# Kernel tuning notes

Hardware: AMD Instinct MI355X
Metric: run time of the kernel (lower is better)

Reference implementation:

```python
import jax, jax.numpy as jnp
import numpy as np

B, S, D = 2, 2048, 1024
E, K, F = 64, 6, 1408
DFF = 4096
N = B * S
CAP = 768
Z_LOSS_W = 1e-6
MOE_SCALE = 0.5  # 1/(1 + (num_shared_experts > 0))


def setup_inputs() -> dict:
    key = jax.random.key(0)
    ks = jax.random.split(key, 7)
    x = jax.random.normal(ks[0], (B, S, D), jnp.float32)
    router_w = jax.random.normal(ks[1], (E, D), jnp.float32) * 0.01
    experts_w12 = jax.random.normal(ks[2], (E, D, 2 * F), jnp.float32) * 0.011
    experts_w3 = jax.random.normal(ks[3], (E, F, D), jnp.float32) * 0.011
    gate_w = jax.random.normal(ks[4], (DFF, D), jnp.float32) * 0.011
    up_w = jax.random.normal(ks[5], (DFF, D), jnp.float32) * 0.011
    down_w = jax.random.normal(ks[6], (D, DFF), jnp.float32) * 0.011
    return {"x": x, "router_w": router_w, "experts_w12": experts_w12,
            "experts_w3": experts_w3, "gate_w": gate_w, "up_w": up_w,
            "down_w": down_w}


def reference(x, router_w, experts_w12, experts_w3, gate_w, up_w, down_w):
    b, s, d = x.shape
    h = x.reshape(-1, d)                    # [N, D]
    n = h.shape[0]

    # ---- router (fp32) ----
    logits = h @ router_w.T                 # [N, E]
    scores = jax.nn.sigmoid(logits)
    z_loss = jnp.mean(logits ** 2) * Z_LOSS_W
    # expert_bias defaults to zeros -> selection on scores directly
    _, topk_idx = jax.lax.top_k(scores, K)  # [N, K]
    topk_idx = jnp.clip(topk_idx, 0, E - 1)
    topk_logits = jnp.take_along_axis(logits, topk_idx, axis=1)
    gating = jax.nn.softmax(topk_logits, axis=-1).astype(jnp.bfloat16)  # [N, K]

    # ---- shared expert (dense SwiGLU) ----
    shared = (jax.nn.silu(h @ gate_w.T) * (h @ up_w.T)) @ down_w.T  # [N, D]

    # ---- dispatch: sort token-expert pairs by expert, scatter into padded buffer ----
    flat_idx = topk_idx.reshape(-1)                     # [N*K]
    order = jnp.argsort(flat_idx)
    expert_sorted = flat_idx[order]                     # [N*K]
    token_ids = jnp.repeat(jnp.arange(n), K)[order]     # source token per pair
    counts = jnp.bincount(flat_idx, length=E)
    starts = jnp.concatenate([jnp.zeros((1,), counts.dtype), jnp.cumsum(counts)[:-1]])
    intra = jnp.arange(n * K) - starts[expert_sorted]   # slot within expert
    valid = intra < CAP
    dest = jnp.where(valid, expert_sorted * CAP + intra, E * CAP)  # overflow -> trash row

    grouped = h[token_ids]                              # [N*K, D]
    padded = jnp.zeros((E * CAP + 1, d), h.dtype).at[dest].set(grouped)
    padded = padded[:-1].reshape(E, CAP, d)             # [E, CAP, D]

    # ---- per-expert grouped GEMM (SwiGLU) ----
    h12 = jnp.einsum('ecd,edf->ecf', padded, experts_w12)   # [E, CAP, 2F]
    h1, h2 = jnp.split(h12, 2, axis=-1)
    act = jax.nn.silu(h1) * h2
    eout = jnp.einsum('ecf,efd->ecd', act, experts_w3)      # [E, CAP, D]

    # ---- combine: gather back and scatter-add into token order ----
    eout_flat = jnp.concatenate([eout.reshape(-1, d), jnp.zeros((1, d), eout.dtype)])
    full = eout_flat[dest]                              # [N*K, D]
    g_sorted = gating.reshape(-1)[order].astype(h.dtype)
    weighted = full * g_sorted[:, None]
    routed = jnp.zeros((n, d), h.dtype).at[token_ids].add(weighted)

    # eval mode: aux_loss = 0, route_scale = 1.0
    out = (shared + routed) * MOE_SCALE
    return out.reshape(b, s, d), z_loss
```

## Files before the change

### kernel.cpp

```cpp
#include <hip/hip_runtime.h>
#include <stdint.h>
#include <math.h>

#define NTOK 4096
#define DIM  1024
#define NEXP 64
#define KSEL 6
#define FF   1408
#define FF2  2816
#define DFFC 4096
#define CAPE 768

typedef __bf16 bf16x8 __attribute__((ext_vector_type(8)));
typedef float  f32x4  __attribute__((ext_vector_type(4)));

__device__ __forceinline__ float bf2f(uint32_t h) {
  union { uint32_t u; float f; } v; v.u = h << 16; return v.f;
}
__device__ __forceinline__ uint16_t f2bf(float f) {
  union { float f; uint32_t u; } v; v.f = f;
  return (uint16_t)((v.u + 0x7fffu + ((v.u >> 16) & 1u)) >> 16);
}
__device__ __forceinline__ uint32_t pk_bf16(float a, float b) {
  uint32_t r;
  asm("v_cvt_pk_bf16_f32 %0, %1, %2" : "=v"(r) : "v"(a), "v"(b));
  return r;
}
__device__ __forceinline__ int swzh(int r) { return ((r ^ (r >> 2)) & 7) << 3; }

__device__ __forceinline__ void load_lds16(const void* g, void* l) {
  __builtin_amdgcn_global_load_lds((const __attribute__((address_space(1))) void*)g,
                                   (__attribute__((address_space(3))) void*)l, 16, 0, 0);
}

__global__ __launch_bounds__(256) void router_kernel(const float* __restrict__ x,
                                                     const float* __restrict__ rw,
                                                     int* __restrict__ topk,
                                                     uint16_t* __restrict__ gating,
                                                     float* __restrict__ tokz,
                                                     uint16_t* __restrict__ hb) {
  __shared__ float hs[16 * DIM];
  __shared__ float lg[16][NEXP];
  const int tid = threadIdx.x;
  const int t0 = blockIdx.x * 16;
  const float4* xin = (const float4*)(x + (size_t)t0 * DIM);
  float4* hs4 = (float4*)hs;
  for (int i = tid; i < 16 * DIM / 4; i += 256) hs4[i] = xin[i];
  __syncthreads();
  {
    ushort4* hbo = (ushort4*)(hb + (size_t)t0 * DIM);
    for (int i = tid; i < 16 * DIM / 4; i += 256) {
      float4 v = hs4[i];
      ushort4 o;
      o.x = f2bf(v.x); o.y = f2bf(v.y); o.z = f2bf(v.z); o.w = f2bf(v.w);
      hbo[i] = o;
    }
  }
  const int e = tid >> 2, q = tid & 3;
  float part[16];
#pragma unroll
  for (int tt = 0; tt < 16; tt++) part[tt] = 0.f;
  const float4* rw4 = (const float4*)(rw + (size_t)e * DIM + q * 256);
  for (int i = 0; i < 64; i++) {
    float4 w = rw4[i];
#pragma unroll
    for (int tt = 0; tt < 16; tt++) {
      float4 h = *(const float4*)(hs + tt * DIM + q * 256 + i * 4);
      part[tt] += h.x * w.x + h.y * w.y + h.z * w.z + h.w * w.w;
    }
  }
#pragma unroll
  for (int tt = 0; tt < 16; tt++) {
    float v = part[tt];
    v += __shfl_xor(v, 1);
    v += __shfl_xor(v, 2);
    if (q == 0) lg[tt][e] = v;
  }
  __syncthreads();
  const int wid = tid >> 6, lane = tid & 63;
  for (int ti = 0; ti < 4; ti++) {
    int tt = wid * 4 + ti;
    float v = lg[tt][lane];
    float z = v * v;
#pragma unroll
    for (int off = 32; off; off >>= 1) z += __shfl_xor(z, off);
    float bv[KSEL]; int bi[KSEL];
#pragma unroll
    for (int s = 0; s < KSEL; s++) {
      float m = v; int mi = lane;
#pragma unroll
      for (int off = 32; off; off >>= 1) {
        float om = __shfl_xor(m, off); int oi = __shfl_xor(mi, off);
        if (om > m || (om == m && oi < mi)) { m = om; mi = oi; }
      }
      bv[s] = m; bi[s] = mi;
      if (lane == mi) v = -3.0e38f;
    }
    if (lane == 0) {
      int t = t0 + tt;
      tokz[t] = z;
      float mx = bv[0];
      float ex[KSEL], sum = 0.f;
#pragma unroll
      for (int s = 0; s < KSEL; s++) { ex[s] = expf(bv[s] - mx); sum += ex[s]; }
      float inv = 1.f / sum;
#pragma unroll
      for (int s = 0; s < KSEL; s++) {
        topk[t * KSEL + s] = bi[s];
        gating[t * KSEL + s] = f2bf(ex[s] * inv);
      }
    }
  }
}

__global__ __launch_bounds__(256) void zred_kernel(const float* __restrict__ tz,
                                                   float* __restrict__ out) {
  __shared__ float s[256];
  float a = 0.f;
  for (int i = threadIdx.x; i < NTOK; i += 256) a += tz[i];
  s[threadIdx.x] = a; __syncthreads();
  for (int st = 128; st; st >>= 1) {
    if (threadIdx.x < (unsigned)st) s[threadIdx.x] += s[threadIdx.x + st];
    __syncthreads();
  }
  if (threadIdx.x == 0) out[0] = s[0] * (1e-6f / ((float)NTOK * (float)NEXP));
}

__global__ __launch_bounds__(64) void dispatch_kernel(const int* __restrict__ topk,
                                                      int* __restrict__ dest,
                                                      int* __restrict__ invmap,
                                                      int* __restrict__ counts) {
  const int e = blockIdx.x;
  const int lane = threadIdx.x;
  int base = 0;
  for (int it = 0; it < (NTOK * KSEL) / 64; it++) {
    int p = it * 64 + lane;
    int ex = topk[p];
    bool m = (ex == e);
    unsigned long long mask = __ballot(m);
    if (m) {
      int intra = base + __popcll(mask & ((1ull << lane) - 1ull));
      if (intra < CAPE) {
        dest[p] = e * CAPE + intra;
        invmap[e * CAPE + intra] = p / KSEL;
      } else {
        dest[p] = -1;
      }
    }
    base += __popcll(mask);
  }
  if (lane == 0) counts[e] = base < CAPE ? base : CAPE;
}

#define BM 128
#define BN 128
#define BKK 64

template<int EPI, int BSRC, bool IND, bool REMAP>
__global__ __launch_bounds__(256, 3) void gemm_f(const uint16_t* __restrict__ A,
                                                 const float* __restrict__ B,
                                                 const float* __restrict__ B2,
                                                 void* __restrict__ C,
                                                 const int* __restrict__ invmap,
                                                 const int* __restrict__ counts,
                                                 int K, int lda, int ldb, int ldc,
                                                 long long strideA, long long strideB,
                                                 long long strideC, int grouped,
                                                 int nM, int nN) {
  const int per = gridDim.x >> 3;
  const int w = ((int)blockIdx.x & 7) * per + ((int)blockIdx.x >> 3);
  const int mi = w % nM;
  const int q1 = w / nM;
  const int ni = q1 % nN;
  const int e  = q1 / nN;
  int cnt = 1 << 30;
  if (grouped) {
    cnt = counts[e];
    if (mi * BM >= cnt) return;
  }
  const int bm0 = mi * BM, bn0 = ni * BN;
  const uint16_t* Ab = A + (size_t)e * strideA;
  const float* Bb = B + (size_t)e * strideB;
  __shared__ alignas(16) uint16_t sA[2][BM * BKK];
  __shared__ alignas(16) uint16_t sB[BN * BKK];
  const int tid = threadIdx.x, wid = tid >> 6, lane = tid & 63;

  const int sa = tid >> 3;
  const int colk = (((tid & 7) ^ ((sa ^ (sa >> 2)) & 7)) * 8);
  const uint16_t* ap[4];
#pragma unroll
  for (int i = 0; i < 4; i++) {
    int row = i * 32 + sa;
    int ar = bm0 + row;
    if constexpr (IND) {
      int cr = ar < cnt ? ar : (cnt - 1);
      ar = invmap[e * CAPE + cr];
    }
    ap[i] = Ab + (size_t)ar * lda + colk;
  }

  const float* bpa = nullptr;
  const float* bpb = nullptr;
  if constexpr (BSRC == 1) {
    const int kc = (tid & 15) * 4;
    bpa = Bb + (size_t)(bn0 + (tid >> 4)) * ldb + kc;
  } else if constexpr (BSRC == 3) {
    const int kc = (tid & 15) * 4;
    const int gcol = (bn0 >> 1) + (tid >> 4);
    bpa = B  + (size_t)gcol * ldb + kc;
    bpb = B2 + (size_t)gcol * ldb + kc;
  } else {
    const int n0 = 4 * (tid & 31);
    int vn0 = bn0 + n0;
    int ng0;
    if constexpr (REMAP) {
      int blk = vn0 >> 5, lo = vn0 & 31;
      ng0 = blk * 16 + (lo & 15) + (lo < 16 ? 0 : FF);
    } else {
      ng0 = vn0;
    }
    bpa = Bb + (size_t)(4 * (tid >> 5)) * ldb + ng0;
  }

  auto loadB = [&](f32x4 (&v)[8]) {
    if constexpr (BSRC == 1) {
#pragma unroll
      for (int it = 0; it < 8; it++)
        v[it] = *(const f32x4*)(bpa + (size_t)(it * 16) * ldb);
      bpa += BKK;
    } else if constexpr (BSRC == 3) {
#pragma unroll
      for (int it = 0; it < 8; it++) {
        const float* s = (it & 1) ? bpb : bpa;
        v[it] = *(const f32x4*)(s + (size_t)((it >> 1) * 16) * ldb);
      }
      bpa += BKK; bpb += BKK;
    } else {
#pragma unroll
      for (int i2 = 0; i2 < 2; i2++)
#pragma unroll
        for (int j = 0; j < 4; j++)
          v[i2 * 4 + j] = *(const f32x4*)(bpa + (size_t)(32 * i2 + j) * ldb);
      bpa += (size_t)BKK * ldb;
    }
  };
  auto issueA = [&](int buf) {
#pragma unroll
    for (int i = 0; i < 4; i++) {
      load_lds16(ap[i], sA[buf] + i * 2048 + wid * 512);
      ap[i] += BKK;
    }
  };
  auto writeB = [&](f32x4 (&v)[8]) {
    if constexpr (BSRC == 1 || BSRC == 3) {
      const int kc = (tid & 15) * 4;
#pragma unroll
      for (int it = 0; it < 8; it++) {
        int nr = (tid >> 4) + it * 16;
        uint2 p;
        p.x = pk_bf16(v[it][0], v[it][1]);
        p.y = pk_bf16(v[it][2], v[it][3]);
        *(uint2*)(sB + nr * BKK + (kc ^ swzh(nr))) = p;
      }
    } else {
      const int n0 = 4 * (tid & 31);
#pragma unroll
      for (int i2 = 0; i2 < 2; i2++) {
        int kk0 = 4 * (tid >> 5) + 32 * i2;
#pragma unroll
        for (int c = 0; c < 4; c++) {
          int nr = n0 + c;
          uint2 p;
          p.x = pk_bf16(v[i2 * 4 + 0][c], v[i2 * 4 + 1][c]);
          p.y = pk_bf16(v[i2 * 4 + 2][c], v[i2 * 4 + 3][c]);
          *(uint2*)(sB + nr * BKK + (kk0 ^ swzh(nr))) = p;
        }
      }
    }
  };

  f32x4 zero = {0.f, 0.f, 0.f, 0.f};
  f32x4 acc[4][4];
#pragma unroll
  for (int i = 0; i < 4; i++)
#pragma unroll
    for (int j = 0; j < 4; j++) acc[i][j] = zero;
  const int wm = wid >> 1, wn = wid & 1;

  f32x4 bv[8];
  issueA(0);
  loadB(bv);

  const int T = K / BKK;
  for (int t = 0; t < T; t++) {
    const int cur = t & 1, nb = cur ^ 1;
    const bool more = (t + 1 < T);
    if (more) issueA(nb);
    writeB(bv);
    if (more) loadB(bv);
    asm volatile("s_waitcnt lgkmcnt(0)" ::: "memory");
    __builtin_amdgcn_sched_barrier(0);
    __builtin_amdgcn_s_barrier();
    __builtin_amdgcn_sched_barrier(0);
#pragma unroll
    for (int ks = 0; ks < 2; ks++) {
      const int kb = ks * 32 + (lane >> 4) * 8;
      bf16x8 af[4], bfr[4];
#pragma unroll
      for (int f = 0; f < 4; f++) {
        int rowA = wm * 64 + f * 16 + (lane & 15);
        af[f] = *(const bf16x8*)(sA[cur] + rowA * BKK + (kb ^ swzh(rowA)));
      }
#pragma unroll
      for (int f = 0; f < 4; f++) {
        int rowB = wn * 64 + f * 16 + (lane & 15);
        bfr[f] = *(const bf16x8*)(sB + rowB * BKK + (kb ^ swzh(rowB)));
      }
#pragma unroll
      for (int fm = 0; fm < 4; fm++)
#pragma unroll
        for (int fn = 0; fn < 4; fn++)
          acc[fm][fn] = __builtin_amdgcn_mfma_f32_16x16x32_bf16(af[fm], bfr[fn],
                                                                acc[fm][fn], 0, 0, 0);
    }
    __builtin_amdgcn_sched_barrier(0);
    __builtin_amdgcn_s_barrier();
    __builtin_amdgcn_sched_barrier(0);
  }

  const int lr = (lane >> 4) * 4, lc = lane & 15;
  if constexpr (EPI == 2) {
    uint16_t* outp = (uint16_t*)C + (size_t)e * strideC;
#pragma unroll
    for (int fm = 0; fm < 4; fm++) {
#pragma unroll
      for (int fp = 0; fp < 2; fp++) {
        f32x4 g = acc[fm][2 * fp], u = acc[fm][2 * fp + 1];
        int fcol = (bn0 >> 1) + wn * 32 + fp * 16 + lc;
#pragma unroll
        for (int j = 0; j < 4; j++) {
          int r = bm0 + wm * 64 + fm * 16 + lr + j;
          float gv = g[j];
          float sv = (gv / (1.f + expf(-gv))) * u[j];
          outp[(size_t)r * ldc + fcol] = f2bf(sv);
        }
      }
    }
  } else if constexpr (EPI == 1) {
    float* outp = (float*)C + (size_t)e * strideC;
#pragma unroll
    for (int fm = 0; fm < 4; fm++)
#pragma unroll
      for (int fn = 0; fn < 4; fn++) {
        int col = bn0 + wn * 64 + fn * 16 + lc;
#pragma unroll
        for (int j = 0; j < 4; j++) {
          int r = bm0 + wm * 64 + fm * 16 + lr + j;
          outp[(size_t)r * ldc + col] = acc[fm][fn][j];
        }
      }
  } else {
    uint16_t* outp = (uint16_t*)C + (size_t)e * strideC;
#pragma unroll
    for (int fm = 0; fm < 4; fm++)
#pragma unroll
      for (int fn = 0; fn < 4; fn++) {
        int col = bn0 + wn * 64 + fn * 16 + lc;
#pragma unroll
        for (int j = 0; j < 4; j++) {
          int r = bm0 + wm * 64 + fm * 16 + lr + j;
          outp[(size_t)r * ldc + col] = f2bf(acc[fm][fn][j]);
        }
      }
  }
}

__global__ __launch_bounds__(256) void combine_kernel(const float* __restrict__ shout,
                                                      const uint16_t* __restrict__ eout,
                                                      const int* __restrict__ dest,
                                                      const uint16_t* __restrict__ gating,
                                                      float* __restrict__ out) {
  const int t = blockIdx.x;
  const int d0 = threadIdx.x * 4;
  float4 s0 = *(const float4*)(shout + (size_t)t * DIM + d0);
  float4 s1 = *(const float4*)(shout + (size_t)NTOK * DIM + (size_t)t * DIM + d0);
  float rx = 0.f, ry = 0.f, rz = 0.f, rw = 0.f;
#pragma unroll
  for (int k = 0; k < KSEL; k++) {
    int dp = dest[t * KSEL + k];
    if (dp >= 0) {
      float gw = bf2f(gating[t * KSEL + k]);
      ushort4 ev = *(const ushort4*)(eout + (size_t)dp * DIM + d0);
      rx += gw * bf2f(ev.x);
      ry += gw * bf2f(ev.y);
      rz += gw * bf2f(ev.z);
      rw += gw * bf2f(ev.w);
    }
  }
  float4 o;
  o.x = (s0.x + s1.x + rx) * 0.5f;
  o.y = (s0.y + s1.y + ry) * 0.5f;
  o.z = (s0.z + s1.z + rz) * 0.5f;
  o.w = (s0.w + s1.w + rw) * 0.5f;
  *(float4*)(out + (size_t)t * DIM + d0) = o;
}

extern "C" void kernel_launch(void* const* d_in, const int* in_sizes, int n_in,
                              void* d_out, int out_size, void* d_ws, size_t ws_size,
                              hipStream_t stream) {
  (void)in_sizes; (void)n_in; (void)out_size; (void)ws_size;
  const float* x   = (const float*)d_in[0];
  const float* rw  = (const float*)d_in[1];
  const float* w12 = (const float*)d_in[2];
  const float* w3  = (const float*)d_in[3];
  const float* gw  = (const float*)d_in[4];
  const float* uw  = (const float*)d_in[5];
  const float* dw  = (const float*)d_in[6];
  float* out = (float*)d_out;

  char* ws = (char*)d_ws;
  size_t off = 0;
  auto alloc = [&](size_t sz) -> void* {
    void* p = ws + off;
    off += (sz + 255) & ~(size_t)255;
    return p;
  };
  uint16_t* HB    = (uint16_t*)alloc((size_t)NTOK * DIM * 2);
  uint16_t* S1    = (uint16_t*)alloc((size_t)NTOK * DFFC * 2);
  uint16_t* ACT   = (uint16_t*)alloc((size_t)NEXP * CAPE * FF * 2);
  uint16_t* EOUT  = (uint16_t*)alloc((size_t)NEXP * CAPE * DIM * 2);
  float* SHOUT    = (float*)alloc((size_t)2 * NTOK * DIM * 4);
  int* TOPKB      = (int*)alloc((size_t)NTOK * KSEL * 4);
  uint16_t* GATING= (uint16_t*)alloc((size_t)NTOK * KSEL * 2);
  int* DEST       = (int*)alloc((size_t)NTOK * KSEL * 4);
  int* INVMAP     = (int*)alloc((size_t)NEXP * CAPE * 4);
  int* COUNTS     = (int*)alloc((size_t)NEXP * 4);
  float* TOKZ     = (float*)alloc((size_t)NTOK * 4);

  router_kernel<<<NTOK / 16, 256, 0, stream>>>(x, rw, TOPKB, GATING, TOKZ, HB);
  dispatch_kernel<<<NEXP, 64, 0, stream>>>(TOPKB, DEST, INVMAP, COUNTS);
  zred_kernel<<<1, 256, 0, stream>>>(TOKZ, out + (size_t)NTOK * DIM);

  gemm_f<2, 3, false, false><<<(NTOK / BM) * (2 * DFFC / BN), 256, 0, stream>>>(
      HB, gw, uw, S1, nullptr, nullptr, DIM, DIM, DIM, DFFC, 0, 0, 0, 0,
      NTOK / BM, 2 * DFFC / BN);
  gemm_f<1, 1, false, false><<<(NTOK / BM) * (DIM / BN) * 2, 256, 0, stream>>>(
      S1, dw, nullptr, SHOUT, nullptr, nullptr, DFFC / 2, DFFC, DFFC, DIM,
      DFFC / 2, DFFC / 2, (long long)NTOK * DIM, 0, NTOK / BM, DIM / BN);

  gemm_f<2, 2, true, true><<<(CAPE / BM) * (FF2 / BN) * NEXP, 256, 0, stream>>>(
      HB, w12, nullptr, ACT, INVMAP, COUNTS, DIM, DIM, FF2, FF,
      0, (long long)DIM * FF2, (long long)CAPE * FF, 1, CAPE / BM, FF2 / BN);
  gemm_f<0, 2, false, false><<<(CAPE / BM) * (DIM / BN) * NEXP, 256, 0, stream>>>(
      ACT, w3, nullptr, EOUT, nullptr, COUNTS, FF, FF, DIM, DIM,
      (long long)CAPE * FF, (long long)FF * DIM, (long long)CAPE * DIM, 1,
      CAPE / BM, DIM / BN);

  combine_kernel<<<NTOK, 256, 0, stream>>>(SHOUT, EOUT, DEST, GATING, out);
}
```

Measured before the change: 758.8 us.

## Double-buffer B tile in LDS and cut to one barrier per k-step

Doubles the shared-memory B tile so the next k-step's A and B tiles are written while the current one is consumed by MFMAs. B global loads now run two steps ahead, and each iteration ends with a single barrier that waits with a partial vmcnt instead of two full barriers. The aim is to hide global-load and LDS-write latency and remove one synchronization per iteration. The cost is 16KB more LDS per block and the removal of the minimum-occupancy hint, so the register budget and occupancy may change.

```diff
diff --git a/kernel.cpp b/kernel.cpp
--- a/kernel.cpp
+++ b/kernel.cpp
@@ -157,16 +157,16 @@
 #define BKK 64
 
 template<int EPI, int BSRC, bool IND, bool REMAP>
-__global__ __launch_bounds__(256, 3) void gemm_f(const uint16_t* __restrict__ A,
-                                                 const float* __restrict__ B,
-                                                 const float* __restrict__ B2,
-                                                 void* __restrict__ C,
-                                                 const int* __restrict__ invmap,
-                                                 const int* __restrict__ counts,
-                                                 int K, int lda, int ldb, int ldc,
-                                                 long long strideA, long long strideB,
-                                                 long long strideC, int grouped,
-                                                 int nM, int nN) {
+__global__ __launch_bounds__(256) void gemm_f(const uint16_t* __restrict__ A,
+                                              const float* __restrict__ B,
+                                              const float* __restrict__ B2,
+                                              void* __restrict__ C,
+                                              const int* __restrict__ invmap,
+                                              const int* __restrict__ counts,
+                                              int K, int lda, int ldb, int ldc,
+                                              long long strideA, long long strideB,
+                                              long long strideC, int grouped,
+                                              int nM, int nN) {
   const int per = gridDim.x >> 3;
   const int w = ((int)blockIdx.x & 7) * per + ((int)blockIdx.x >> 3);
   const int mi = w % nM;
@@ -182,7 +182,7 @@
   const uint16_t* Ab = A + (size_t)e * strideA;
   const float* Bb = B + (size_t)e * strideB;
   __shared__ alignas(16) uint16_t sA[2][BM * BKK];
-  __shared__ alignas(16) uint16_t sB[BN * BKK];
+  __shared__ alignas(16) uint16_t sB[2][BN * BKK];
   const int tid = threadIdx.x, wid = tid >> 6, lane = tid & 63;
 
   const int sa = tid >> 3;
@@ -251,7 +251,7 @@
       ap[i] += BKK;
     }
   };
-  auto writeB = [&](f32x4 (&v)[8]) {
+  auto writeB = [&](int buf, f32x4 (&v)[8]) {
     if constexpr (BSRC == 1 || BSRC == 3) {
       const int kc = (tid & 15) * 4;
 #pragma unroll
@@ -260,7 +260,7 @@
         uint2 p;
         p.x = pk_bf16(v[it][0], v[it][1]);
         p.y = pk_bf16(v[it][2], v[it][3]);
-        *(uint2*)(sB + nr * BKK + (kc ^ swzh(nr))) = p;
+        *(uint2*)(sB[buf] + nr * BKK + (kc ^ swzh(nr))) = p;
       }
     } else {
       const int n0 = 4 * (tid & 31);
@@ -273,7 +273,7 @@
           uint2 p;
           p.x = pk_bf16(v[i2 * 4 + 0][c], v[i2 * 4 + 1][c]);
           p.y = pk_bf16(v[i2 * 4 + 2][c], v[i2 * 4 + 3][c]);
-          *(uint2*)(sB + nr * BKK + (kk0 ^ swzh(nr))) = p;
+          *(uint2*)(sB[buf] + nr * BKK + (kk0 ^ swzh(nr))) = p;
         }
       }
     }
@@ -287,21 +287,26 @@
     for (int j = 0; j < 4; j++) acc[i][j] = zero;
   const int wm = wid >> 1, wn = wid & 1;
 
+  const int T = K / BKK;
   f32x4 bv[8];
   issueA(0);
   loadB(bv);
-
-  const int T = K / BKK;
+  writeB(0, bv);
+  if (T > 1) loadB(bv);
+  asm volatile("s_waitcnt lgkmcnt(0)" ::: "memory");
+  __builtin_amdgcn_sched_barrier(0);
+  __builtin_amdgcn_s_barrier();
+  __builtin_amdgcn_sched_barrier(0);
+
   for (int t = 0; t < T; t++) {
     const int cur = t & 1, nb = cur ^ 1;
-    const bool more = (t + 1 < T);
-    if (more) issueA(nb);
-    writeB(bv);
-    if (more) loadB(bv);
-    asm volatile("s_waitcnt lgkmcnt(0)" ::: "memory");
-    __builtin_amdgcn_sched_barrier(0);
-    __builtin_amdgcn_s_barrier();
-    __builtin_amdgcn_sched_barrier(0);
+    const bool more1 = (t + 1 < T);
+    const bool more2 = (t + 2 < T);
+    if (more1) {
+      issueA(nb);
+      writeB(nb, bv);
+    }
+    if (more2) loadB(bv);
 #pragma unroll
     for (int ks = 0; ks < 2; ks++) {
       const int kb = ks * 32 + (lane >> 4) * 8;
@@ -314,7 +319,7 @@
 #pragma unroll
       for (int f = 0; f < 4; f++) {
         int rowB = wn * 64 + f * 16 + (lane & 15);
-        bfr[f] = *(const bf16x8*)(sB + rowB * BKK + (kb ^ swzh(rowB)));
+        bfr[f] = *(const bf16x8*)(sB[cur] + rowB * BKK + (kb ^ swzh(rowB)));
       }
 #pragma unroll
       for (int fm = 0; fm < 4; fm++)
@@ -323,9 +328,16 @@
           acc[fm][fn] = __builtin_amdgcn_mfma_f32_16x16x32_bf16(af[fm], bfr[fn],
                                                                 acc[fm][fn], 0, 0, 0);
     }
-    __builtin_amdgcn_sched_barrier(0);
-    __builtin_amdgcn_s_barrier();
-    __builtin_amdgcn_sched_barrier(0);
+    if (more1) {
+      if (more2) {
+        asm volatile("s_waitcnt vmcnt(8) lgkmcnt(0)" ::: "memory");
+      } else {
+        asm volatile("s_waitcnt vmcnt(0) lgkmcnt(0)" ::: "memory");
+      }
+      __builtin_amdgcn_sched_barrier(0);
+      __builtin_amdgcn_s_barrier();
+      __builtin_amdgcn_sched_barrier(0);
+    }
   }
 
   const int lr = (lane >> 4) * 4, lc = lane & 15;
```

New measurement: 845.9 us. 1.11x slower.

## Merge shared and routed expert GEMMs into combined launches, fold z-loss into dispatch

Applied to the files above, without the earlier changes.

The shared-expert up GEMM and the routed-expert w12 GEMM now run in one launch, with the block index deciding which problem each block handles. The two down GEMMs are merged the same way. The z-loss reduction becomes an extra block of the dispatch kernel. This removes launch gaps and the tail underutilisation at the end of each GEMM, so the grouped GEMM's sparse and early-exiting blocks can overlap with dense shared-expert work. The cost is that both template bodies share one kernel's register budget and occupancy.

```diff
diff --git a/kernel.cpp b/kernel.cpp
--- a/kernel.cpp
+++ b/kernel.cpp
@@ -113,25 +113,22 @@
   }
 }
 
-__global__ __launch_bounds__(256) void zred_kernel(const float* __restrict__ tz,
-                                                   float* __restrict__ out) {
-  __shared__ float s[256];
-  float a = 0.f;
-  for (int i = threadIdx.x; i < NTOK; i += 256) a += tz[i];
-  s[threadIdx.x] = a; __syncthreads();
-  for (int st = 128; st; st >>= 1) {
-    if (threadIdx.x < (unsigned)st) s[threadIdx.x] += s[threadIdx.x + st];
-    __syncthreads();
-  }
-  if (threadIdx.x == 0) out[0] = s[0] * (1e-6f / ((float)NTOK * (float)NEXP));
-}
-
 __global__ __launch_bounds__(64) void dispatch_kernel(const int* __restrict__ topk,
                                                       int* __restrict__ dest,
                                                       int* __restrict__ invmap,
-                                                      int* __restrict__ counts) {
+                                                      int* __restrict__ counts,
+                                                      const float* __restrict__ tz,
+                                                      float* __restrict__ zout) {
+  const int lane = threadIdx.x;
+  if (blockIdx.x == NEXP) {
+    float a = 0.f;
+    for (int i = lane; i < NTOK; i += 64) a += tz[i];
+#pragma unroll
+    for (int off = 32; off; off >>= 1) a += __shfl_xor(a, off);
+    if (lane == 0) zout[0] = a * (1e-6f / ((float)NTOK * (float)NEXP));
+    return;
+  }
   const int e = blockIdx.x;
-  const int lane = threadIdx.x;
   int base = 0;
   for (int it = 0; it < (NTOK * KSEL) / 64; it++) {
     int p = it * 64 + lane;
@@ -156,34 +153,33 @@
 #define BN 128
 #define BKK 64
 
+struct GArgs {
+  const uint16_t* A; const float* B; const float* B2; void* C;
+  const int* invmap; const int* counts;
+  int K, lda, ldb, ldc;
+  long long strideA, strideB, strideC;
+  int grouped, nM, nN, nblk;
+};
+
 template<int EPI, int BSRC, bool IND, bool REMAP>
-__global__ __launch_bounds__(256, 3) void gemm_f(const uint16_t* __restrict__ A,
-                                                 const float* __restrict__ B,
-                                                 const float* __restrict__ B2,
-                                                 void* __restrict__ C,
-                                                 const int* __restrict__ invmap,
-                                                 const int* __restrict__ counts,
-                                                 int K, int lda, int ldb, int ldc,
-                                                 long long strideA, long long strideB,
-                                                 long long strideC, int grouped,
-                                                 int nM, int nN) {
-  const int per = gridDim.x >> 3;
-  const int w = ((int)blockIdx.x & 7) * per + ((int)blockIdx.x >> 3);
-  const int mi = w % nM;
-  const int q1 = w / nM;
-  const int ni = q1 % nN;
-  const int e  = q1 / nN;
+__device__ __forceinline__ void gemm_body(const GArgs& g, int bid,
+                                          uint16_t* sAbase, uint16_t* sB) {
+  const int per = g.nblk >> 3;
+  const int w = (bid & 7) * per + (bid >> 3);
+  const int mi = w % g.nM;
+  const int q1 = w / g.nM;
+  const int ni = q1 % g.nN;
+  const int e  = q1 / g.nN;
   int cnt = 1 << 30;
-  if (grouped) {
-    cnt = counts[e];
+  if (g.grouped) {
+    cnt = g.counts[e];
     if (mi * BM >= cnt) return;
   }
   const int bm0 = mi * BM, bn0 = ni * BN;
-  const uint16_t* Ab = A + (size_t)e * strideA;
-  const float* Bb = B + (size_t)e * strideB;
-  __shared__ alignas(16) uint16_t sA[2][BM * BKK];
-  __shared__ alignas(16) uint16_t sB[BN * BKK];
+  const uint16_t* Ab = g.A + (size_t)e * g.strideA;
+  const float* Bb = g.B + (size_t)e * g.strideB;
   const int tid = threadIdx.x, wid = tid >> 6, lane = tid & 63;
+  const int lda = g.lda, ldb = g.ldb, ldc = g.ldc;
 
   const int sa = tid >> 3;
   const int colk = (((tid & 7) ^ ((sa ^ (sa >> 2)) & 7)) * 8);
@@ -194,7 +190,7 @@
     int ar = bm0 + row;
     if constexpr (IND) {
       int cr = ar < cnt ? ar : (cnt - 1);
-      ar = invmap[e * CAPE + cr];
+      ar = g.invmap[e * CAPE + cr];
     }
     ap[i] = Ab + (size_t)ar * lda + colk;
   }
@@ -207,8 +203,8 @@
   } else if constexpr (BSRC == 3) {
     const int kc = (tid & 15) * 4;
     const int gcol = (bn0 >> 1) + (tid >> 4);
-    bpa = B  + (size_t)gcol * ldb + kc;
-    bpb = B2 + (size_t)gcol * ldb + kc;
+    bpa = g.B  + (size_t)gcol * ldb + kc;
+    bpb = g.B2 + (size_t)gcol * ldb + kc;
   } else {
     const int n0 = 4 * (tid & 31);
     int vn0 = bn0 + n0;
@@ -247,7 +243,7 @@
   auto issueA = [&](int buf) {
 #pragma unroll
     for (int i = 0; i < 4; i++) {
-      load_lds16(ap[i], sA[buf] + i * 2048 + wid * 512);
+      load_lds16(ap[i], sAbase + buf * (BM * BKK) + i * 2048 + wid * 512);
       ap[i] += BKK;
     }
   };
@@ -291,7 +287,7 @@
   issueA(0);
   loadB(bv);
 
-  const int T = K / BKK;
+  const int T = g.K / BKK;
   for (int t = 0; t < T; t++) {
     const int cur = t & 1, nb = cur ^ 1;
     const bool more = (t + 1 < T);
@@ -309,7 +305,7 @@
 #pragma unroll
       for (int f = 0; f < 4; f++) {
         int rowA = wm * 64 + f * 16 + (lane & 15);
-        af[f] = *(const bf16x8*)(sA[cur] + rowA * BKK + (kb ^ swzh(rowA)));
+        af[f] = *(const bf16x8*)(sAbase + cur * (BM * BKK) + rowA * BKK + (kb ^ swzh(rowA)));
       }
 #pragma unroll
       for (int f = 0; f < 4; f++) {
@@ -330,24 +326,24 @@
 
   const int lr = (lane >> 4) * 4, lc = lane & 15;
   if constexpr (EPI == 2) {
-    uint16_t* outp = (uint16_t*)C + (size_t)e * strideC;
+    uint16_t* outp = (uint16_t*)g.C + (size_t)e * g.strideC;
 #pragma unroll
     for (int fm = 0; fm < 4; fm++) {
 #pragma unroll
       for (int fp = 0; fp < 2; fp++) {
-        f32x4 g = acc[fm][2 * fp], u = acc[fm][2 * fp + 1];
+        f32x4 gg = acc[fm][2 * fp], u = acc[fm][2 * fp + 1];
         int fcol = (bn0 >> 1) + wn * 32 + fp * 16 + lc;
 #pragma unroll
         for (int j = 0; j < 4; j++) {
           int r = bm0 + wm * 64 + fm * 16 + lr + j;
-          float gv = g[j];
+          float gv = gg[j];
           float sv = (gv / (1.f + expf(-gv))) * u[j];
           outp[(size_t)r * ldc + fcol] = f2bf(sv);
         }
       }
     }
   } else if constexpr (EPI == 1) {
-    float* outp = (float*)C + (size_t)e * strideC;
+    float* outp = (float*)g.C + (size_t)e * g.strideC;
 #pragma unroll
     for (int fm = 0; fm < 4; fm++)
 #pragma unroll
@@ -360,7 +356,7 @@
         }
       }
   } else {
-    uint16_t* outp = (uint16_t*)C + (size_t)e * strideC;
+    uint16_t* outp = (uint16_t*)g.C + (size_t)e * g.strideC;
 #pragma unroll
     for (int fm = 0; fm < 4; fm++)
 #pragma unroll
@@ -373,6 +369,21 @@
         }
       }
   }
+}
+
+__global__ __launch_bounds__(256, 3) void fused_up(GArgs a, GArgs b) {
+  __shared__ alignas(16) uint16_t sA[2][BM * BKK];
+  __shared__ alignas(16) uint16_t sB[BN * BKK];
+  const int bid = blockIdx.x;
+  if (bid < a.nblk) gemm_body<2, 3, false, false>(a, bid, &sA[0][0], sB);
+  else              gemm_body<2, 2, true,  true >(b, bid - a.nblk, &sA[0][0], sB);
+}
+__global__ __launch_bounds__(256, 3) void fused_down(GArgs a, GArgs b) {
+  __shared__ alignas(16) uint16_t sA[2][BM * BKK];
+  __shared__ alignas(16) uint16_t sB[BN * BKK];
+  const int bid = blockIdx.x;
+  if (bid < a.nblk) gemm_body<1, 1, false, false>(a, bid, &sA[0][0], sB);
+  else              gemm_body<0, 2, false, false>(b, bid - a.nblk, &sA[0][0], sB);
 }
 
 __global__ __launch_bounds__(256) void combine_kernel(const float* __restrict__ shout,
@@ -438,23 +449,25 @@
   float* TOKZ     = (float*)alloc((size_t)NTOK * 4);
 
   router_kernel<<<NTOK / 16, 256, 0, stream>>>(x, rw, TOPKB, GATING, TOKZ, HB);
-  dispatch_kernel<<<NEXP, 64, 0, stream>>>(TOPKB, DEST, INVMAP, COUNTS);
-  zred_kernel<<<1, 256, 0, stream>>>(TOKZ, out + (size_t)NTOK * DIM);
-
-  gemm_f<2, 3, false, false><<<(NTOK / BM) * (2 * DFFC / BN), 256, 0, stream>>>(
-      HB, gw, uw, S1, nullptr, nullptr, DIM, DIM, DIM, DFFC, 0, 0, 0, 0,
-      NTOK / BM, 2 * DFFC / BN);
-  gemm_f<1, 1, false, false><<<(NTOK / BM) * (DIM / BN) * 2, 256, 0, stream>>>(
-      S1, dw, nullptr, SHOUT, nullptr, nullptr, DFFC / 2, DFFC, DFFC, DIM,
-      DFFC / 2, DFFC / 2, (long long)NTOK * DIM, 0, NTOK / BM, DIM / BN);
-
-  gemm_f<2, 2, true, true><<<(CAPE / BM) * (FF2 / BN) * NEXP, 256, 0, stream>>>(
-      HB, w12, nullptr, ACT, INVMAP, COUNTS, DIM, DIM, FF2, FF,
-      0, (long long)DIM * FF2, (long long)CAPE * FF, 1, CAPE / BM, FF2 / BN);
-  gemm_f<0, 2, false, false><<<(CAPE / BM) * (DIM / BN) * NEXP, 256, 0, stream>>>(
-      ACT, w3, nullptr, EOUT, nullptr, COUNTS, FF, FF, DIM, DIM,
-      (long long)CAPE * FF, (long long)FF * DIM, (long long)CAPE * DIM, 1,
-      CAPE / BM, DIM / BN);
+  dispatch_kernel<<<NEXP + 1, 64, 0, stream>>>(TOPKB, DEST, INVMAP, COUNTS,
+                                               TOKZ, out + (size_t)NTOK * DIM);
+
+  GArgs gup = { HB, gw, uw, S1, nullptr, nullptr,
+                DIM, DIM, DIM, DFFC, 0, 0, 0,
+                0, NTOK / BM, 2 * DFFC / BN, (NTOK / BM) * (2 * DFFC / BN) };
+  GArgs g12 = { HB, w12, nullptr, ACT, INVMAP, COUNTS,
+                DIM, DIM, FF2, FF, 0, (long long)DIM * FF2, (long long)CAPE * FF,
+                1, CAPE / BM, FF2 / BN, (CAPE / BM) * (FF2 / BN) * NEXP };
+  fused_up<<<gup.nblk + g12.nblk, 256, 0, stream>>>(gup, g12);
+
+  GArgs gdn = { S1, dw, nullptr, SHOUT, nullptr, nullptr,
+                DFFC / 2, DFFC, DFFC, DIM, DFFC / 2, DFFC / 2, (long long)NTOK * DIM,
+                0, NTOK / BM, DIM / BN, (NTOK / BM) * (DIM / BN) * 2 };
+  GArgs gw3 = { ACT, w3, nullptr, EOUT, nullptr, COUNTS,
+                FF, FF, DIM, DIM, (long long)CAPE * FF, (long long)FF * DIM,
+                (long long)CAPE * DIM, 1, CAPE / BM, DIM / BN,
+                (CAPE / BM) * (DIM / BN) * NEXP };
+  fused_down<<<gdn.nblk + gw3.nblk, 256, 0, stream>>>(gdn, gw3);
 
   combine_kernel<<<NTOK, 256, 0, stream>>>(SHOUT, EOUT, DEST, GATING, out);
 }
```

Measured after the change: 731.1 us (median of 2 runs). 3.7% less time.
